# Kernel optimization log

Measured on AMD Instinct MI355X. Metric: run time of the kernel, lower is better.

## Reference

```python
import jax, jax.numpy as jnp
import numpy as np

B, S, D, H = 8, 512, 1024, 16
DH = D // H
GAMMA = 0.1      # kl_gamma
KL_EPS = 1e-10
LN_EPS = 1e-5
SCALE = 1.0 / np.sqrt(DH).astype(np.float32)


def setup_inputs() -> dict:
    key = jax.random.key(0)
    ks = iter(jax.random.split(key, 32))
    rnd = lambda shape, s: jax.random.normal(next(ks), shape, jnp.float32) * s
    inp = {
        'title_features': rnd((B, S, D), 1.0),
        'content_features': rnd((B, S, D), 1.0),
    }
    for pre in ('t2c', 'c2t'):
        # small Q/K weights + bias 1.0 keep row-means of scores positive (log is defined)
        inp[pre + '_wq'] = rnd((D, D), 0.02); inp[pre + '_bq'] = jnp.ones((D,), jnp.float32)
        inp[pre + '_wk'] = rnd((D, D), 0.02); inp[pre + '_bk'] = jnp.ones((D,), jnp.float32)
        inp[pre + '_wv'] = rnd((D, D), 0.02); inp[pre + '_bv'] = jnp.zeros((D,), jnp.float32)
        inp[pre + '_wo'] = rnd((D, D), 0.02); inp[pre + '_bo'] = jnp.zeros((D,), jnp.float32)
    inp['gate_w'] = rnd((2 * D, D), 0.02)
    inp['gate_b'] = jnp.zeros((D,), jnp.float32)
    inp['ln_g'] = jnp.ones((D,), jnp.float32)
    inp['ln_b'] = jnpps = jnp.zeros((D,), jnp.float32)
    inp['ln_b'] = jnp.zeros((D,), jnp.float32)
    return inp


def _daa(q_in, k_in, v_in, wq, bq, wk, bk, wv, bv, wo, bo):
    """DivergenceAlignedAttention forward (eval mode, use_uniform_target=False)."""
    Bq, Sq, _ = q_in.shape
    Sk = k_in.shape[1]
    Q = (q_in @ wq + bq).reshape(Bq, Sq, H, DH)
    K = (k_in @ wk + bk).reshape(Bq, Sk, H, DH)
    V = (v_in @ wv + bv).reshape(Bq, Sk, H, DH)
    scores = jnp.einsum('bqhd,bkhd->bhqk', Q, K) * SCALE           # [B,H,Sq,Sk]
    tgt = jnp.mean(scores, axis=-1, keepdims=True)                 # row mean
    scores = scores + GAMMA * jnp.log(tgt + KL_EPS)                # fused KL term
    attn = jax.nn.softmax(scores, axis=-1)
    ctx = jnp.einsum('bhqk,bkhd->bqhd', attn, V).reshape(Bq, Sq, D)
    return ctx @ wo + bo


def _layer_norm(x, g, b):
    mu = jnp.mean(x, axis=-1, keepdims=True)
    var = jnp.mean(jnp.square(x - mu), axis=-1, keepdims=True)
    return g * (x - mu) / jnp.sqrt(var + LN_EPS) + b


def reference(title_features, content_features,
              t2c_wq, t2c_bq, t2c_wk, t2c_bk, t2c_wv, t2c_bv, t2c_wo, t2c_bo,
              c2t_wq, c2t_bq, c2t_wk, c2t_bk, c2t_wv, c2t_bv, c2t_wo, c2t_bo,
              gate_w, gate_b, ln_g, ln_b):
    t2c = _daa(content_features, title_features, title_features,
               t2c_wq, t2c_bq, t2c_wk, t2c_bk, t2c_wv, t2c_bv, t2c_wo, t2c_bo)
    c2t = _daa(title_features, content_features, content_features,
               c2t_wq, c2t_bq, c2t_wk, c2t_bk, c2t_wv, c2t_bv, c2t_wo, c2t_bo)
    gate_t = jax.nn.sigmoid(jnp.concatenate([title_features, t2c], axis=-1) @ gate_w + gate_b)
    gate_c = jax.nn.sigmoid(jnp.concatenate([content_features, c2t], axis=-1) @ gate_w + gate_b)
    fused_title = _layer_norm(gate_t * title_features + (1.0 - gate_t) * t2c, ln_g, ln_b)
    fused_content = _layer_norm(gate_c * content_features + (1.0 - gate_c) * c2t, ln_g, ln_b)
    return (fused_title, fused_content)
```

## Files before the change

### kernel.cpp

```cpp
#include <hip/hip_runtime.h>
#include <cstdint>
#include <cstddef>

typedef unsigned short ushort_t;
typedef unsigned int u32;
typedef __attribute__((ext_vector_type(8))) short bf16x8;
typedef __attribute__((ext_vector_type(4))) float f32x4;
typedef __attribute__((ext_vector_type(4))) unsigned short u16x4;

#define DEV static __device__ __forceinline__

DEV ushort_t f2bf(float f) {
  u32 x = __float_as_uint(f);
  x += 0x7fff + ((x >> 16) & 1);
  return (ushort_t)(x >> 16);
}
DEV float bf2f(ushort_t u) { return __uint_as_float(((u32)u) << 16); }

DEV void gload16(const ushort_t* g, ushort_t* l) {
  __builtin_amdgcn_global_load_lds(
      (const __attribute__((address_space(1))) void*)g,
      (__attribute__((address_space(3))) void*)l, 16, 0, 0);
}


__global__ __launch_bounds__(256) void cvt_inputs(
    const float* __restrict__ xa, const float* __restrict__ xb,
    ushort_t* __restrict__ oa, ushort_t* __restrict__ ob) {
  int i = blockIdx.x * 256 + threadIdx.x;
  f32x4 va = ((const f32x4*)xa)[i];
  f32x4 vb = ((const f32x4*)xb)[i];
  u16x4 ua, ub;
#pragma unroll
  for (int j = 0; j < 4; ++j) { ua[j] = f2bf(va[j]); ub[j] = f2bf(vb[j]); }
  ((u16x4*)oa)[i] = ua;
  ((u16x4*)ob)[i] = ub;
}

struct Src9 { const float* p[9]; };

__global__ __launch_bounds__(256) void transpose_cvt(
    Src9 srcs, ushort_t* __restrict__ WTall, ushort_t* __restrict__ WgT) {
  const int z = blockIdx.z;
  const int K = (z == 8) ? 2048 : 1024;
  if (z < 8 && blockIdx.y >= 32) return;
  const float* src = srcs.p[z];
  ushort_t* dst = (z == 8) ? WgT : WTall + ((size_t)z << 20);
  __shared__ float t[32][33];
  int n0 = blockIdx.x << 5, k0 = blockIdx.y << 5;
  int tx = threadIdx.x & 31, ty = threadIdx.x >> 5;
#pragma unroll
  for (int i = 0; i < 4; ++i)
    t[ty + i * 8][tx] = src[(size_t)(k0 + ty + i * 8) * 1024 + n0 + tx];
  __syncthreads();
#pragma unroll
  for (int i = 0; i < 4; ++i)
    dst[(size_t)(n0 + ty + i * 8) * K + k0 + tx] = f2bf(t[tx][ty + i * 8]);
}

enum { M_QKV = 0, M_OUT = 1, M_GATE = 2 };
struct Ptr6 { const float* p[6]; };

template <int MODE>
__global__ __launch_bounds__(256, 3) void gemm_kernel(
    const ushort_t* __restrict__ A1a, const ushort_t* __restrict__ A1b,
    const ushort_t* __restrict__ A2, const ushort_t* __restrict__ Bbase,
    Ptr6 bt, void* __restrict__ out) {
  constexpr int KTOT = (MODE == M_GATE) ? 2048 : 1024;
  __shared__ ushort_t As[128 * 64];
  __shared__ ushort_t Bs[128 * 64];
  const int tid = threadIdx.x;
  const int w = tid >> 6, lane = tid & 63;
  const int g = lane >> 4, c = lane & 15;
  const int wm = (w >> 1) << 6, wn = (w & 1) << 6;
  const int m0 = blockIdx.x << 7, n0 = blockIdx.y << 7;
  const int group = m0 >> 12;
  const int bidx = (MODE == M_QKV) ? group * 3 + (n0 >> 10)
                 : (MODE == M_OUT) ? 6 + group : 0;
  const int csw = (lane & 7) ^ (lane >> 3);

  f32x4 acc[4][4];
#pragma unroll
  for (int i = 0; i < 4; ++i)
#pragma unroll
    for (int j = 0; j < 4; ++j) acc[i][j] = f32x4{0.f, 0.f, 0.f, 0.f};

  for (int k0 = 0; k0 < KTOT; k0 += 64) {
#pragma unroll
    for (int i = 0; i < 4; ++i) {
      const int chunk = (w << 2) + i;
      const int row = (chunk << 3) + (lane >> 3);
      const int mg = m0 + row;
      const ushort_t* ap;
      if (MODE == M_GATE && k0 >= 1024) {
        ap = A2 + ((size_t)mg << 10) + (k0 - 1024) + (csw << 3);
      } else {
        const ushort_t* ab = (MODE == M_OUT)
            ? A1a + ((size_t)mg << 10)
            : ((mg >> 12) ? A1b : A1a) + ((size_t)(mg & 4095) << 10);
        ap = ab + k0 + (csw << 3);
      }
      gload16(ap, &As[(size_t)chunk << 9]);
      const ushort_t* bp;
      if (MODE == M_GATE)
        bp = Bbase + ((size_t)(n0 + row) << 11) + k0 + (csw << 3);
      else
        bp = Bbase + ((size_t)bidx << 20) + ((size_t)((n0 & 1023) + row) << 10) +
             k0 + (csw << 3);
      gload16(bp, &Bs[(size_t)chunk << 9]);
    }
    __syncthreads();
    const int cg = c & 7;
#pragma unroll
    for (int ks = 0; ks < 2; ++ks) {
      bf16x8 af[4], bfr[4];
#pragma unroll
      for (int mi = 0; mi < 4; ++mi)
        af[mi] = *(const bf16x8*)&As[((wm + mi * 16 + c) << 6) +
                                     ((((ks << 2) | g) ^ cg) << 3)];
#pragma unroll
      for (int ni = 0; ni < 4; ++ni)
        bfr[ni] = *(const bf16x8*)&Bs[((wn + ni * 16 + c) << 6) +
                                      ((((ks << 2) | g) ^ cg) << 3)];
#pragma unroll
      for (int mi = 0; mi < 4; ++mi)
#pragma unroll
        for (int ni = 0; ni < 4; ++ni)
          acc[mi][ni] = __builtin_amdgcn_mfma_f32_16x16x32_bf16(
              af[mi], bfr[ni], acc[mi][ni], 0, 0, 0);
    }
    __syncthreads();
  }

#pragma unroll
  for (int ni = 0; ni < 4; ++ni) {
    const int n = n0 + wn + ni * 16 + c;
    float bv;
    if (MODE == M_QKV)      bv = bt.p[bidx][n & 1023];
    else if (MODE == M_OUT) bv = bt.p[group][n];
    else                    bv = bt.p[0][n];
#pragma unroll
    for (int mi = 0; mi < 4; ++mi) {
      const int mb = m0 + wm + mi * 16 + (g << 2);
      f32x4 a = acc[mi][ni];
      if (MODE == M_QKV) {
        const int mrow = mb & 4095, b = mrow >> 9, s = mrow & 511;
        const int nloc = n & 1023, h = nloc >> 6, d = nloc & 63;
        ushort_t* base = (ushort_t*)out + ((size_t)bidx << 22);
        if (bidx == 1 || bidx == 5) {
          u16x4 o;
#pragma unroll
          for (int r = 0; r < 4; ++r) o[r] = f2bf(a[r] + bv);
          *(u16x4*)&base[(((size_t)((b * 16 + h) * 64 + d)) << 9) + s] = o;
        } else {
#pragma unroll
          for (int r = 0; r < 4; ++r)
            base[(((size_t)((b * 16 + h) * 512 + s + r)) << 6) + d] = f2bf(a[r] + bv);
        }
      } else if (MODE == M_OUT) {
#pragma unroll
        for (int r = 0; r < 4; ++r)
          ((ushort_t*)out)[(size_t)(mb + r) * 1024 + n] = f2bf(a[r] + bv);
      } else {
#pragma unroll
        for (int r = 0; r < 4; ++r)
          ((float*)out)[(size_t)(mb + r) * 1024 + n] = a[r] + bv;
      }
    }
  }
}

__global__ __launch_bounds__(256, 2) void attn_kernel(
    const ushort_t* __restrict__ QKV, ushort_t* __restrict__ ctx) {
  __shared__ ushort_t kv[2][8192];
  const int tid = threadIdx.x, w = tid >> 6, lane = tid & 63;
  const int g = lane >> 4, c = lane & 15, c7 = c & 7;
  const int bid = (int)blockIdx.x;
  const int wid = (bid & 7) * 256 + (bid >> 3);
  const int dir = wid >> 10;
  const int bh = (wid >> 3) & 127, qt = wid & 7;
  const int q0 = (qt << 6) + (w << 4);
  const int qs = dir ? 2 : 3, ks = dir ? 4 : 0, vs = dir ? 5 : 1;
  const ushort_t* Qb = QKV + ((size_t)qs << 22) + ((size_t)bh << 15);
  const ushort_t* Kb = QKV + ((size_t)ks << 22) + ((size_t)bh << 15);
  const ushort_t* Vb = QKV + ((size_t)vs << 22) + ((size_t)bh << 15);

  auto stageK = [&](int b, int kc) {
#pragma unroll
    for (int i = 0; i < 4; ++i) {
      int idx = tid + (i << 8);
      int r = idx >> 3, sl = idx & 7;
      int cs = sl ^ (r & 7);
      gload16(Kb + (((size_t)((kc << 7) + r)) << 6) + (cs << 3), &kv[b][idx << 3]);
    }
  };
  auto stageV = [&](int b, int vc) {
#pragma unroll
    for (int i = 0; i < 4; ++i) {
      int idx = tid + (i << 8);
      int r = idx >> 4, sl = idx & 15;
      int cs = sl ^ (r & 15);
      gload16(Vb + ((size_t)r << 9) + (vc << 7) + (cs << 3), &kv[b][idx << 3]);
    }
  };

  bf16x8 qf0 = *(const bf16x8*)&Qb[((q0 + c) << 6) + (g << 3)];
  bf16x8 qf1 = *(const bf16x8*)&Qb[((q0 + c) << 6) + 32 + (g << 3)];

  f32x4 s[32];
  float mx = -1e30f;
  int buf = 0;
  stageK(0, 0);
  __syncthreads();
#pragma unroll
  for (int kc = 0; kc < 4; ++kc) {
    if (kc < 3) stageK(buf ^ 1, kc + 1);
    __builtin_amdgcn_s_setprio(1);
#pragma unroll
    for (int t = 0; t < 8; ++t) {
      const ushort_t* base = &kv[buf][((t << 4) + c) << 6];
      bf16x8 a0 = *(const bf16x8*)&base[(g ^ c7) << 3];
      bf16x8 a1 = *(const bf16x8*)&base[((4 | g) ^ c7) << 3];
      f32x4 z = {0.f, 0.f, 0.f, 0.f};
      z = __builtin_amdgcn_mfma_f32_16x16x32_bf16(a0, qf0, z, 0, 0, 0);
      z = __builtin_amdgcn_mfma_f32_16x16x32_bf16(a1, qf1, z, 0, 0, 0);
      s[kc * 8 + t] = z;
      mx = fmaxf(mx, fmaxf(fmaxf(z[0], z[1]), fmaxf(z[2], z[3])));
    }
    __builtin_amdgcn_s_setprio(0);
    __syncthreads();
    buf ^= 1;
  }
  stageV(0, 0);
  buf = 0;

  mx = fmaxf(mx, __shfl_xor(mx, 16, 64));
  mx = fmaxf(mx, __shfl_xor(mx, 32, 64));
  const float SC = 0.125f;
  float sum = 0.f;
#pragma unroll
  for (int t = 0; t < 32; ++t) {
#pragma unroll
    for (int r = 0; r < 4; ++r) {
      float p = __expf((s[t][r] - mx) * SC);
      s[t][r] = p;
      sum += p;
    }
  }
  sum += __shfl_xor(sum, 16, 64);
  sum += __shfl_xor(sum, 32, 64);
  const float inv = 1.0f / sum;

  f32x4 pacc[4];
#pragma unroll
  for (int dt = 0; dt < 4; ++dt) pacc[dt] = f32x4{0.f, 0.f, 0.f, 0.f};
  const int s1 = ((g & 1) << 5) + c;
  const int s2 = s1 + 16;
  const bool hi = (g >> 1) != 0;
  __syncthreads();
#pragma unroll
  for (int vc = 0; vc < 4; ++vc) {
    if (vc < 3) stageV(buf ^ 1, vc + 1);
#pragma unroll
    for (int t2l = 0; t2l < 4; ++t2l) {
      const int t2 = (vc << 2) + t2l;
      u32 A0 = ((u32)f2bf(s[2 * t2][1]) << 16) | f2bf(s[2 * t2][0]);
      u32 A1p = ((u32)f2bf(s[2 * t2][3]) << 16) | f2bf(s[2 * t2][2]);
      u32 B0 = ((u32)f2bf(s[2 * t2 + 1][1]) << 16) | f2bf(s[2 * t2 + 1][0]);
      u32 B1 = ((u32)f2bf(s[2 * t2 + 1][3]) << 16) | f2bf(s[2 * t2 + 1][2]);
      u32 xA0 = (u32)__shfl((int)A0, s1, 64), xA1 = (u32)__shfl((int)A1p, s1, 64);
      u32 xB0 = (u32)__shfl((int)B0, s1, 64), xB1 = (u32)__shfl((int)B1, s1, 64);
      u32 yA0 = (u32)__shfl((int)A0, s2, 64), yA1 = (u32)__shfl((int)A1p, s2, 64);
      u32 yB0 = (u32)__shfl((int)B0, s2, 64), yB1 = (u32)__shfl((int)B1, s2, 64);
      union { bf16x8 v; u32 wd[4]; } pb;
      pb.wd[0] = hi ? xB0 : xA0;
      pb.wd[1] = hi ? xB1 : xA1;
      pb.wd[2] = hi ? yB0 : yA0;
      pb.wd[3] = hi ? yB1 : yA1;
      __builtin_amdgcn_s_setprio(1);
#pragma unroll
      for (int dt = 0; dt < 4; ++dt) {
        bf16x8 av = *(const bf16x8*)
            &kv[buf][(((dt << 4) + c) << 7) + ((((t2l << 2) | g) ^ c) << 3)];
        pacc[dt] = __builtin_amdgcn_mfma_f32_16x16x32_bf16(av, pb.v, pacc[dt], 0, 0, 0);
      }
      __builtin_amdgcn_s_setprio(0);
    }
    __syncthreads();
    buf ^= 1;
  }

  const int b = bh >> 4, h = bh & 15;
  size_t obase = ((size_t)dir << 22) + ((size_t)(b * 512 + q0 + c) << 10) + (h << 6);
#pragma unroll
  for (int dt = 0; dt < 4; ++dt) {
    u16x4 o;
#pragma unroll
    for (int r = 0; r < 4; ++r) o[r] = f2bf(pacc[dt][r] * inv);
    *(u16x4*)&ctx[obase + (dt << 4) + (g << 2)] = o;
  }
}

__global__ __launch_bounds__(256) void fuse_ln(
    const float* __restrict__ xt, const float* __restrict__ xc,
    const ushort_t* __restrict__ ao, const float* __restrict__ gl,
    const float* __restrict__ lng, const float* __restrict__ lnb,
    float* __restrict__ out) {
  const int row = blockIdx.x, dir = row >> 12, r = row & 4095;
  const float* x = (dir ? xc : xt) + ((size_t)r << 10);
  const ushort_t* a = ao + ((size_t)row << 10);
  const float* glr = gl + ((size_t)row << 10);
  float* o = out + ((size_t)row << 10);
  const int t = threadIdx.x, w = t >> 6, lane = t & 63;
  f32x4 xv = ((const f32x4*)x)[t];
  u16x4 av = ((const u16x4*)a)[t];
  f32x4 gv = ((const f32x4*)glr)[t];
  f32x4 f;
  float sm = 0.f, sq = 0.f;
#pragma unroll
  for (int j = 0; j < 4; ++j) {
    float gate = 1.f / (1.f + __expf(-gv[j]));
    float fv = gate * xv[j] + (1.f - gate) * bf2f(av[j]);
    f[j] = fv; sm += fv; sq += fv * fv;
  }
#pragma unroll
  for (int d = 1; d < 64; d <<= 1) {
    sm += __shfl_xor(sm, d, 64);
    sq += __shfl_xor(sq, d, 64);
  }
  __shared__ float ps[8];
  if (lane == 0) { ps[w] = sm; ps[4 + w] = sq; }
  __syncthreads();
  sm = ps[0] + ps[1] + ps[2] + ps[3];
  sq = ps[4] + ps[5] + ps[6] + ps[7];
  const float mu = sm * (1.f / 1024.f);
  const float var = sq * (1.f / 1024.f) - mu * mu;
  const float rstd = rsqrtf(var + 1e-5f);
  f32x4 lg = ((const f32x4*)lng)[t], lb = ((const f32x4*)lnb)[t];
  f32x4 ov;
#pragma unroll
  for (int j = 0; j < 4; ++j) ov[j] = lg[j] * (f[j] - mu) * rstd + lb[j];
  ((f32x4*)o)[t] = ov;
}

extern "C" void kernel_launch(void* const* d_in, const int* in_sizes, int n_in,
                              void* d_out, int out_size, void* d_ws, size_t ws_size,
                              hipStream_t stream) {
  (void)in_sizes; (void)n_in; (void)out_size; (void)ws_size;
  const float* title = (const float*)d_in[0];
  const float* content = (const float*)d_in[1];

  char* ws = (char*)d_ws;
  const size_t MB = 1u << 20;
  ushort_t* Xt    = (ushort_t*)(ws + 0 * MB);
  ushort_t* Xc    = (ushort_t*)(ws + 8 * MB);
  ushort_t* WTall = (ushort_t*)(ws + 16 * MB);
  ushort_t* WgT   = (ushort_t*)(ws + 32 * MB);
  ushort_t* QKV   = (ushort_t*)(ws + 36 * MB);
  ushort_t* ao    = (ushort_t*)(ws + 36 * MB);
  float*    gl    = (float*)  (ws + 52 * MB);
  ushort_t* ctx   = (ushort_t*)(ws + 84 * MB);

  cvt_inputs<<<4096, 256, 0, stream>>>(title, content, Xt, Xc);

  Src9 srcs;
  srcs.p[0] = (const float*)d_in[4];  srcs.p[1] = (const float*)d_in[6];
  srcs.p[2] = (const float*)d_in[10]; srcs.p[3] = (const float*)d_in[2];
  srcs.p[4] = (const float*)d_in[12]; srcs.p[5] = (const float*)d_in[14];
  srcs.p[6] = (const float*)d_in[8];  srcs.p[7] = (const float*)d_in[16];
  srcs.p[8] = (const float*)d_in[18];
  transpose_cvt<<<dim3(32, 64, 9), 256, 0, stream>>>(srcs, WTall, WgT);

  Ptr6 bq;
  bq.p[0] = (const float*)d_in[5];  bq.p[1] = (const float*)d_in[7];
  bq.p[2] = (const float*)d_in[11]; bq.p[3] = (const float*)d_in[3];
  bq.p[4] = (const float*)d_in[13]; bq.p[5] = (const float*)d_in[15];
  gemm_kernel<M_QKV><<<dim3(64, 24), 256, 0, stream>>>(Xt, Xc, nullptr, WTall, bq, QKV);

  attn_kernel<<<2048, 256, 0, stream>>>(QKV, ctx);

  Ptr6 bo;
  bo.p[0] = (const float*)d_in[9]; bo.p[1] = (const float*)d_in[17];
  for (int i = 2; i < 6; ++i) bo.p[i] = nullptr;
  gemm_kernel<M_OUT><<<dim3(64, 8), 256, 0, stream>>>(ctx, nullptr, nullptr, WTall, bo, ao);

  Ptr6 bg;
  bg.p[0] = (const float*)d_in[19];
  for (int i = 1; i < 6; ++i) bg.p[i] = nullptr;
  gemm_kernel<M_GATE><<<dim3(64, 8), 256, 0, stream>>>(Xt, Xc, ao, WgT, bg, gl);

  fuse_ln<<<8192, 256, 0, stream>>>(title, content, ao, gl,
                                    (const float*)d_in[20], (const float*)d_in[21],
                                    (float*)d_out);
}
```

Before: 218.4 us.

## Fold output projection into gate weights and use pipelined 256x256 GEMMs

```diff
diff --git a/kernel.cpp b/kernel.cpp
--- a/kernel.cpp
+++ b/kernel.cpp
@@ -22,6 +22,10 @@
       (const __attribute__((address_space(1))) void*)g,
       (__attribute__((address_space(3))) void*)l, 16, 0, 0);
 }
+
+#define VMW(n) asm volatile("s_waitcnt vmcnt(" #n ")" ::: "memory")
+#define LGKM0 asm volatile("s_waitcnt lgkmcnt(0)" ::: "memory")
+#define BAR() __builtin_amdgcn_s_barrier()
 
 
 __global__ __launch_bounds__(256) void cvt_inputs(
@@ -37,18 +41,28 @@
   ((u16x4*)ob)[i] = ub;
 }
 
-struct Src9 { const float* p[9]; };
+struct Src11 { const float* p[11]; };
 
 __global__ __launch_bounds__(256) void transpose_cvt(
-    Src9 srcs, ushort_t* __restrict__ WTall, ushort_t* __restrict__ WgT) {
+    Src11 srcs, ushort_t* __restrict__ WTall, ushort_t* __restrict__ WgT,
+    ushort_t* __restrict__ WoBF) {
   const int z = blockIdx.z;
+  if (z != 8 && blockIdx.y >= 32) return;
+  const float* src = srcs.p[z];
+  int tx = threadIdx.x & 31, ty = threadIdx.x >> 5;
+  int n0 = blockIdx.x << 5, k0 = blockIdx.y << 5;
+  if (z >= 9) {
+    ushort_t* dst = WoBF + ((size_t)(z - 9) << 20);
+#pragma unroll
+    for (int i = 0; i < 4; ++i) {
+      size_t off = (size_t)(k0 + ty + i * 8) * 1024 + n0 + tx;
+      dst[off] = f2bf(src[off]);
+    }
+    return;
+  }
   const int K = (z == 8) ? 2048 : 1024;
-  if (z < 8 && blockIdx.y >= 32) return;
-  const float* src = srcs.p[z];
   ushort_t* dst = (z == 8) ? WgT : WTall + ((size_t)z << 20);
   __shared__ float t[32][33];
-  int n0 = blockIdx.x << 5, k0 = blockIdx.y << 5;
-  int tx = threadIdx.x & 31, ty = threadIdx.x >> 5;
 #pragma unroll
   for (int i = 0; i < 4; ++i)
     t[ty + i * 8][tx] = src[(size_t)(k0 + ty + i * 8) * 1024 + n0 + tx];
@@ -58,15 +72,21 @@
     dst[(size_t)(n0 + ty + i * 8) * K + k0 + tx] = f2bf(t[tx][ty + i * 8]);
 }
 
-enum { M_QKV = 0, M_OUT = 1, M_GATE = 2 };
-struct Ptr6 { const float* p[6]; };
-
-template <int MODE>
-__global__ __launch_bounds__(256, 3) void gemm_kernel(
-    const ushort_t* __restrict__ A1a, const ushort_t* __restrict__ A1b,
-    const ushort_t* __restrict__ A2, const ushort_t* __restrict__ Bbase,
-    Ptr6 bt, void* __restrict__ out) {
-  constexpr int KTOT = (MODE == M_GATE) ? 2048 : 1024;
+__global__ __launch_bounds__(256) void gb2_kernel(
+    const float* __restrict__ bo0, const float* __restrict__ bo1,
+    const ushort_t* __restrict__ WgT, float* __restrict__ gb2) {
+  int idx = blockIdx.x * 256 + threadIdx.x;
+  int dir = idx >> 10, n = idx & 1023;
+  const float* bo = dir ? bo1 : bo0;
+  const ushort_t* wrow = WgT + ((size_t)n << 11) + 1024;
+  float s = 0.f;
+  for (int k = 0; k < 1024; ++k) s += bo[k] * bf2f(wrow[k]);
+  gb2[idx] = s;
+}
+
+__global__ __launch_bounds__(256, 3) void gemm_wp(
+    const ushort_t* __restrict__ WgT, const ushort_t* __restrict__ WoBF,
+    ushort_t* __restrict__ WpT) {
   __shared__ ushort_t As[128 * 64];
   __shared__ ushort_t Bs[128 * 64];
   const int tid = threadIdx.x;
@@ -74,9 +94,7 @@
   const int g = lane >> 4, c = lane & 15;
   const int wm = (w >> 1) << 6, wn = (w & 1) << 6;
   const int m0 = blockIdx.x << 7, n0 = blockIdx.y << 7;
-  const int group = m0 >> 12;
-  const int bidx = (MODE == M_QKV) ? group * 3 + (n0 >> 10)
-                 : (MODE == M_OUT) ? 6 + group : 0;
+  const int group = m0 >> 10;
   const int csw = (lane & 7) ^ (lane >> 3);
 
   f32x4 acc[4][4];
@@ -85,29 +103,15 @@
 #pragma unroll
     for (int j = 0; j < 4; ++j) acc[i][j] = f32x4{0.f, 0.f, 0.f, 0.f};
 
-  for (int k0 = 0; k0 < KTOT; k0 += 64) {
+  for (int k0 = 0; k0 < 1024; k0 += 64) {
 #pragma unroll
     for (int i = 0; i < 4; ++i) {
       const int chunk = (w << 2) + i;
       const int row = (chunk << 3) + (lane >> 3);
-      const int mg = m0 + row;
-      const ushort_t* ap;
-      if (MODE == M_GATE && k0 >= 1024) {
-        ap = A2 + ((size_t)mg << 10) + (k0 - 1024) + (csw << 3);
-      } else {
-        const ushort_t* ab = (MODE == M_OUT)
-            ? A1a + ((size_t)mg << 10)
-            : ((mg >> 12) ? A1b : A1a) + ((size_t)(mg & 4095) << 10);
-        ap = ab + k0 + (csw << 3);
-      }
-      gload16(ap, &As[(size_t)chunk << 9]);
-      const ushort_t* bp;
-      if (MODE == M_GATE)
-        bp = Bbase + ((size_t)(n0 + row) << 11) + k0 + (csw << 3);
-      else
-        bp = Bbase + ((size_t)bidx << 20) + ((size_t)((n0 & 1023) + row) << 10) +
-             k0 + (csw << 3);
-      gload16(bp, &Bs[(size_t)chunk << 9]);
+      gload16(WgT + ((size_t)((m0 + row) & 1023) << 11) + 1024 + k0 + (csw << 3),
+              &As[(size_t)chunk << 9]);
+      gload16(WoBF + ((size_t)group << 20) + ((size_t)(n0 + row) << 10) + k0 + (csw << 3),
+              &Bs[(size_t)chunk << 9]);
     }
     __syncthreads();
     const int cg = c & 7;
@@ -131,40 +135,187 @@
     }
     __syncthreads();
   }
-
 #pragma unroll
   for (int ni = 0; ni < 4; ++ni) {
     const int n = n0 + wn + ni * 16 + c;
-    float bv;
-    if (MODE == M_QKV)      bv = bt.p[bidx][n & 1023];
-    else if (MODE == M_OUT) bv = bt.p[group][n];
-    else                    bv = bt.p[0][n];
 #pragma unroll
     for (int mi = 0; mi < 4; ++mi) {
       const int mb = m0 + wm + mi * 16 + (g << 2);
       f32x4 a = acc[mi][ni];
-      if (MODE == M_QKV) {
-        const int mrow = mb & 4095, b = mrow >> 9, s = mrow & 511;
-        const int nloc = n & 1023, h = nloc >> 6, d = nloc & 63;
-        ushort_t* base = (ushort_t*)out + ((size_t)bidx << 22);
-        if (bidx == 1 || bidx == 5) {
-          u16x4 o;
-#pragma unroll
-          for (int r = 0; r < 4; ++r) o[r] = f2bf(a[r] + bv);
-          *(u16x4*)&base[(((size_t)((b * 16 + h) * 64 + d)) << 9) + s] = o;
+#pragma unroll
+      for (int r = 0; r < 4; ++r)
+        WpT[((size_t)group << 20) + ((size_t)((mb + r) & 1023) << 10) + n] = f2bf(a[r]);
+    }
+  }
+}
+
+enum { G_QKV = 0, G_OG = 1 };
+struct Bias8 { const float* p[8]; };
+
+#define RD_A(Q)                                                                \
+  _Pragma("unroll") for (int m2 = 0; m2 < 2; ++m2)                             \
+    _Pragma("unroll") for (int kk = 0; kk < 2; ++kk)                           \
+      af[m2][kk] = *(const bf16x8*)&As[buf][(((wm << 7) + (((Q)*2 + m2) << 4) + c) << 6) + \
+                                           ((((kk << 2) | g) ^ c7) << 3)]
+#define MM(Q)                                                                  \
+  _Pragma("unroll") for (int m2 = 0; m2 < 2; ++m2)                             \
+    _Pragma("unroll") for (int nf = 0; nf < 4; ++nf) {                         \
+      acc[(Q)*2 + m2][nf] = __builtin_amdgcn_mfma_f32_16x16x32_bf16(           \
+          af[m2][0], bfr[nf][0], acc[(Q)*2 + m2][nf], 0, 0, 0);                \
+      acc[(Q)*2 + m2][nf] = __builtin_amdgcn_mfma_f32_16x16x32_bf16(           \
+          af[m2][1], bfr[nf][1], acc[(Q)*2 + m2][nf], 0, 0, 0);                \
+    }
+
+#define GTILE(T_, ST_, V0_, V1_, V2_, V3_)                                     \
+  do {                                                                         \
+    const int buf = (T_)&1;                                                    \
+    const int ko = ((T_) + 1) << 6;                                            \
+    bf16x8 af[2][2];                                                           \
+    VMW(V0_); BAR();                                                           \
+    _Pragma("unroll") for (int nf = 0; nf < 4; ++nf)                           \
+      _Pragma("unroll") for (int kk = 0; kk < 2; ++kk)                         \
+        bfr[nf][kk] = *(const bf16x8*)&Bs[buf][(((wn << 6) + (nf << 4) + c) << 6) + \
+                                              ((((kk << 2) | g) ^ c7) << 3)];  \
+    RD_A(0);                                                                   \
+    if (ST_) stageB(buf ^ 1, ko, 0);                                           \
+    BAR(); LGKM0;                                                              \
+    __builtin_amdgcn_s_setprio(1); MM(0); __builtin_amdgcn_s_setprio(0);       \
+    VMW(V1_); BAR();                                                           \
+    RD_A(1);                                                                   \
+    if (ST_) stageB(buf ^ 1, ko, 1);                                           \
+    BAR(); LGKM0;                                                              \
+    __builtin_amdgcn_s_setprio(1); MM(1); __builtin_amdgcn_s_setprio(0);       \
+    VMW(V2_); BAR();                                                           \
+    RD_A(2);                                                                   \
+    if (ST_) { stageA(buf ^ 1, ko, 0); stageA(buf ^ 1, ko, 1); }               \
+    BAR(); LGKM0;                                                              \
+    __builtin_amdgcn_s_setprio(1); MM(2); __builtin_amdgcn_s_setprio(0);       \
+    VMW(V3_); BAR();                                                           \
+    RD_A(3);                                                                   \
+    if (ST_) { stageA(buf ^ 1, ko, 2); stageA(buf ^ 1, ko, 3); }               \
+    BAR(); LGKM0;                                                              \
+    __builtin_amdgcn_s_setprio(1); MM(3); __builtin_amdgcn_s_setprio(0);       \
+  } while (0)
+
+template <int MODE>
+__global__ __launch_bounds__(512, 2) void gemm256(
+    const ushort_t* __restrict__ Aa, const ushort_t* __restrict__ Ab,
+    const ushort_t* __restrict__ WTall, const ushort_t* __restrict__ WgT,
+    const ushort_t* __restrict__ WpT, Bias8 bt,
+    ushort_t* __restrict__ outQ, ushort_t* __restrict__ gl) {
+  __shared__ ushort_t As[2][16384];
+  __shared__ ushort_t Bs[2][16384];
+  const int tid = threadIdx.x;
+  const int wid = tid >> 6, lane = tid & 63;
+  const int g = lane >> 4, c = lane & 15, c7 = c & 7;
+  const int wm = wid >> 2, wn = wid & 3;
+  constexpr int NB = (MODE == G_QKV) ? 512 : 256;
+  const int bid = (int)blockIdx.x;
+  const int wk = (bid & 7) * (NB >> 3) + (bid >> 3);
+  const int mt = wk & 31, nt = wk >> 5;
+  const int m0 = mt << 8, n0 = nt << 8;
+  const int group = m0 >> 12;
+  const int nch = n0 >> 10;
+
+  const ushort_t* Asrc = (MODE == G_QKV)
+      ? (group ? Ab : Aa) + ((size_t)(m0 & 4095) << 10)
+      : Aa + ((size_t)m0 << 10);
+
+  const ushort_t* Bbase;
+  int bstride, bidx = -1;
+  if (MODE == G_QKV) {
+    if (nch < 3) {
+      bidx = group * 3 + nch;
+      Bbase = WTall + ((size_t)bidx << 20) + ((size_t)(n0 & 1023) << 10);
+      bstride = 1024;
+    } else {
+      Bbase = WgT + ((size_t)(n0 & 1023) << 11);
+      bstride = 2048;
+    }
+  } else {
+    if (nch == 0) {
+      Bbase = WTall + ((size_t)(6 + group) << 20) + ((size_t)n0 << 10);
+      bstride = 1024;
+    } else {
+      Bbase = WpT + ((size_t)group << 20) + ((size_t)(n0 & 1023) << 10);
+      bstride = 1024;
+    }
+  }
+
+  auto stageB = [&](int bf_, int ko, int h) {
+#pragma unroll
+    for (int i = 0; i < 2; ++i) {
+      int rl = (i << 6) + (wid << 3) + (lane >> 3);
+      int row = (h << 7) + rl;
+      int cs = (lane & 7) ^ (lane >> 3);
+      gload16(Bbase + (size_t)row * bstride + ko + (cs << 3),
+              &Bs[bf_][(h << 13) + (i << 12) + (wid << 9)]);
+    }
+  };
+  auto stageA = [&](int bf_, int ko, int q) {
+    int rl = (wid << 3) + (lane >> 3);
+    int row = (q << 5) + (rl & 31) + ((rl & 32) << 2);
+    int cs = (lane & 7) ^ (lane >> 3);
+    gload16(Asrc + ((size_t)row << 10) + ko + (cs << 3),
+            &As[bf_][((q << 5) + ((wid & 3) << 3) + ((wid >> 2) << 7)) << 6]);
+  };
+
+  f32x4 acc[8][4];
+#pragma unroll
+  for (int i = 0; i < 8; ++i)
+#pragma unroll
+    for (int j = 0; j < 4; ++j) acc[i][j] = f32x4{0.f, 0.f, 0.f, 0.f};
+
+  stageB(0, 0, 0); stageB(0, 0, 1);
+  stageA(0, 0, 0); stageA(0, 0, 1); stageA(0, 0, 2); stageA(0, 0, 3);
+
+  bf16x8 bfr[4][2];
+  for (int t = 0; t < 15; ++t) GTILE(t, 1, 3, 4, 5, 6);
+  GTILE(15, 0, 3, 2, 1, 0);
+
+  const float* bp_ = (MODE == G_QKV) ? (nch < 3 ? bt.p[bidx] : bt.p[6])
+                                     : (nch == 0 ? bt.p[group] : bt.p[2 + group]);
+#pragma unroll
+  for (int mf = 0; mf < 8; ++mf) {
+    const int mb = m0 + (wm << 7) + (mf << 4) + (g << 2);
+#pragma unroll
+    for (int nf = 0; nf < 4; ++nf) {
+      const int n = n0 + (wn << 6) + (nf << 4) + c;
+      const int nloc = n & 1023;
+      const float bv = bp_[nloc];
+      f32x4 a = acc[mf][nf];
+      if (MODE == G_QKV) {
+        if (nch < 3) {
+          const int mrow = mb & 4095, b = mrow >> 9, s = mrow & 511;
+          const int h = nloc >> 6, d = nloc & 63;
+          ushort_t* base = outQ + ((size_t)bidx << 22);
+          if (bidx == 1 || bidx == 5) {
+            u16x4 o;
+#pragma unroll
+            for (int r = 0; r < 4; ++r) o[r] = f2bf(a[r] + bv);
+            *(u16x4*)&base[(((size_t)((b * 16 + h) * 64 + d)) << 9) + s] = o;
+          } else {
+#pragma unroll
+            for (int r = 0; r < 4; ++r)
+              base[(((size_t)((b * 16 + h) * 512 + s + r)) << 6) + d] = f2bf(a[r] + bv);
+          }
         } else {
 #pragma unroll
           for (int r = 0; r < 4; ++r)
-            base[(((size_t)((b * 16 + h) * 512 + s + r)) << 6) + d] = f2bf(a[r] + bv);
+            gl[((size_t)(mb + r) << 10) + nloc] = f2bf(a[r] + bv);
         }
-      } else if (MODE == M_OUT) {
-#pragma unroll
-        for (int r = 0; r < 4; ++r)
-          ((ushort_t*)out)[(size_t)(mb + r) * 1024 + n] = f2bf(a[r] + bv);
       } else {
-#pragma unroll
-        for (int r = 0; r < 4; ++r)
-          ((float*)out)[(size_t)(mb + r) * 1024 + n] = a[r] + bv;
+        if (nch == 0) {
+#pragma unroll
+          for (int r = 0; r < 4; ++r)
+            outQ[((size_t)(mb + r) << 10) + nloc] = f2bf(a[r] + bv);
+        } else {
+#pragma unroll
+          for (int r = 0; r < 4; ++r) {
+            size_t off = ((size_t)(mb + r) << 10) + nloc;
+            gl[off] = f2bf(a[r] + bv + bf2f(gl[off]));
+          }
+        }
       }
     }
   }
@@ -303,23 +454,23 @@
 
 __global__ __launch_bounds__(256) void fuse_ln(
     const float* __restrict__ xt, const float* __restrict__ xc,
-    const ushort_t* __restrict__ ao, const float* __restrict__ gl,
+    const ushort_t* __restrict__ ao, const ushort_t* __restrict__ gl,
     const float* __restrict__ lng, const float* __restrict__ lnb,
     float* __restrict__ out) {
   const int row = blockIdx.x, dir = row >> 12, r = row & 4095;
   const float* x = (dir ? xc : xt) + ((size_t)r << 10);
   const ushort_t* a = ao + ((size_t)row << 10);
-  const float* glr = gl + ((size_t)row << 10);
+  const ushort_t* glr = gl + ((size_t)row << 10);
   float* o = out + ((size_t)row << 10);
   const int t = threadIdx.x, w = t >> 6, lane = t & 63;
   f32x4 xv = ((const f32x4*)x)[t];
   u16x4 av = ((const u16x4*)a)[t];
-  f32x4 gv = ((const f32x4*)glr)[t];
+  u16x4 gv = ((const u16x4*)glr)[t];
   f32x4 f;
   float sm = 0.f, sq = 0.f;
 #pragma unroll
   for (int j = 0; j < 4; ++j) {
-    float gate = 1.f / (1.f + __expf(-gv[j]));
+    float gate = 1.f / (1.f + __expf(-bf2f(gv[j])));
     float fv = gate * xv[j] + (1.f - gate) * bf2f(av[j]);
     f[j] = fv; sm += fv; sq += fv * fv;
   }
@@ -354,40 +505,45 @@
   const size_t MB = 1u << 20;
   ushort_t* Xt    = (ushort_t*)(ws + 0 * MB);
   ushort_t* Xc    = (ushort_t*)(ws + 8 * MB);
+  ushort_t* ctx   = (ushort_t*)(ws + 0 * MB);
   ushort_t* WTall = (ushort_t*)(ws + 16 * MB);
   ushort_t* WgT   = (ushort_t*)(ws + 32 * MB);
   ushort_t* QKV   = (ushort_t*)(ws + 36 * MB);
   ushort_t* ao    = (ushort_t*)(ws + 36 * MB);
-  float*    gl    = (float*)  (ws + 52 * MB);
-  ushort_t* ctx   = (ushort_t*)(ws + 84 * MB);
+  ushort_t* gl    = (ushort_t*)(ws + 84 * MB);
+  ushort_t* WoBF  = (ushort_t*)(ws + 100 * MB);
+  ushort_t* WpT   = (ushort_t*)(ws + 104 * MB);
+  float*    gb2   = (float*)   (ws + 108 * MB);
 
   cvt_inputs<<<4096, 256, 0, stream>>>(title, content, Xt, Xc);
 
-  Src9 srcs;
+  Src11 srcs;
   srcs.p[0] = (const float*)d_in[4];  srcs.p[1] = (const float*)d_in[6];
   srcs.p[2] = (const float*)d_in[10]; srcs.p[3] = (const float*)d_in[2];
   srcs.p[4] = (const float*)d_in[12]; srcs.p[5] = (const float*)d_in[14];
   srcs.p[6] = (const float*)d_in[8];  srcs.p[7] = (const float*)d_in[16];
   srcs.p[8] = (const float*)d_in[18];
-  transpose_cvt<<<dim3(32, 64, 9), 256, 0, stream>>>(srcs, WTall, WgT);
-
-  Ptr6 bq;
+  srcs.p[9] = (const float*)d_in[8];  srcs.p[10] = (const float*)d_in[16];
+  transpose_cvt<<<dim3(32, 64, 11), 256, 0, stream>>>(srcs, WTall, WgT, WoBF);
+
+  gb2_kernel<<<8, 256, 0, stream>>>((const float*)d_in[9], (const float*)d_in[17],
+                                    WgT, gb2);
+  gemm_wp<<<dim3(16, 8), 256, 0, stream>>>(WgT, WoBF, WpT);
+
+  Bias8 bq;
   bq.p[0] = (const float*)d_in[5];  bq.p[1] = (const float*)d_in[7];
   bq.p[2] = (const float*)d_in[11]; bq.p[3] = (const float*)d_in[3];
   bq.p[4] = (const float*)d_in[13]; bq.p[5] = (const float*)d_in[15];
-  gemm_kernel<M_QKV><<<dim3(64, 24), 256, 0, stream>>>(Xt, Xc, nullptr, WTall, bq, QKV);
+  bq.p[6] = (const float*)d_in[19]; bq.p[7] = nullptr;
+  gemm256<G_QKV><<<512, 512, 0, stream>>>(Xt, Xc, WTall, WgT, WpT, bq, QKV, gl);
 
   attn_kernel<<<2048, 256, 0, stream>>>(QKV, ctx);
 
-  Ptr6 bo;
+  Bias8 bo;
   bo.p[0] = (const float*)d_in[9]; bo.p[1] = (const float*)d_in[17];
-  for (int i = 2; i < 6; ++i) bo.p[i] = nullptr;
-  gemm_kernel<M_OUT><<<dim3(64, 8), 256, 0, stream>>>(ctx, nullptr, nullptr, WTall, bo, ao);
-
-  Ptr6 bg;
-  bg.p[0] = (const float*)d_in[19];
-  for (int i = 1; i < 6; ++i) bg.p[i] = nullptr;
-  gemm_kernel<M_GATE><<<dim3(64, 8), 256, 0, stream>>>(Xt, Xc, ao, WgT, bg, gl);
+  bo.p[2] = gb2; bo.p[3] = gb2 + 1024;
+  for (int i = 4; i < 8; ++i) bo.p[i] = nullptr;
+  gemm256<G_OG><<<256, 512, 0, stream>>>(ctx, nullptr, WTall, WgT, WpT, bo, ao, gl);
 
   fuse_ln<<<8192, 256, 0, stream>>>(title, content, ao, gl,
                                     (const float*)d_in[20], (const float*)d_in[21],
```

Result: slower. 253.2 us (+15.9%).
